# Kernel tuning notes

Hardware: AMD Instinct MI355X
Metric: run time of the kernel (lower is better)

Reference implementation:

```python
import jax, jax.numpy as jnp
import numpy as np

TOPK = 10
HID = 512
RHID = 150
CH = 32


def _gru(x, Wi, Wh, bi, bh):
    """torch nn.GRU (1 layer, batch_first) with gate order r,z,n. x: [B,T,D]."""
    H = Wh.shape[1]
    xi = x @ Wi.T + bi  # [B,T,3H] precompute input projections

    def step(h, xt):
        gh = h @ Wh.T + bh
        r = jax.nn.sigmoid(xt[:, :H] + gh[:, :H])
        z = jax.nn.sigmoid(xt[:, H:2 * H] + gh[:, H:2 * H])
        n = jnp.tanh(xt[:, 2 * H:] + r * gh[:, 2 * H:])
        h_new = (1.0 - z) * n + z * h
        return h_new, h_new

    h0 = jnp.zeros((x.shape[0], H), x.dtype)
    hT, ys = jax.lax.scan(step, h0, jnp.swapaxes(xi, 0, 1))
    return jnp.swapaxes(ys, 0, 1), hT


def reference(window, emb, w_init, w_root, arma_b, Wi1, Wh1, bi1, bh1,
              Wi2, Wh2, bi2, bh2, W_fc, b_fc):
    B, T, N = window.shape
    # --- SingleEmbedding (post-warmup): cosine similarity + per-row top-k ---
    Wn = emb / jnp.clip(jnp.linalg.norm(emb, axis=1, keepdims=True), 1e-8, None)
    A = Wn @ Wn.T
    A = A * (1.0 - jnp.eye(N, dtype=A.dtype))  # fill_diagonal_(0)
    A = jnp.maximum(A, 0.0)                    # clamp(0)
    vals, idx = jax.lax.top_k(A, TOPK)         # [N, TOPK]
    # zero-valued edges kept with weight 0: identical math (zero degree/message contribution)
    src = jnp.repeat(jnp.arange(N), TOPK)      # edge source = row i
    dst = idx.reshape(-1)                      # edge dest = col j
    attr = vals.reshape(-1)
    # --- batch edges over B (offset b*N), then over T (offset t*B*N), as in torch code ---
    boff = jnp.arange(B) * N
    bsrc = (src[None, :] + boff[:, None]).reshape(-1)   # [B*E]
    bdst = (dst[None, :] + boff[:, None]).reshape(-1)
    battr = jnp.tile(attr, B)
    toff = jnp.arange(T) * (B * N)
    fsrc = (bsrc[None, :] + toff[:, None]).reshape(-1)  # [T*B*E]
    fdst = (bdst[None, :] + toff[:, None]).reshape(-1)
    fattr = jnp.tile(battr, T)
    Ntot = B * N * T
    # node layout (b, n, t): flat row = (b*N + n)*T + t  (faithful to torch view order)
    x = jnp.transpose(window, (0, 2, 1)).reshape(Ntot, 1)
    # --- ARMAConv: 1 stack, 1 layer, GELU, gcn_norm without self-loops ---
    deg = jax.ops.segment_sum(fattr, fdst, num_segments=Ntot)
    dinv = jnp.where(deg > 0, jax.lax.rsqrt(jnp.where(deg > 0, deg, 1.0)), 0.0)
    enorm = dinv[fsrc] * fattr * dinv[fdst]
    h = x @ w_init                                            # [Ntot, CH]
    agg = jax.ops.segment_sum(h[fsrc] * enorm[:, None], fdst, num_segments=Ntot)
    out = jax.nn.gelu(agg + x @ w_root + arma_b, approximate=False)
    # --- add node embedding, GRU encode ---
    xt = out.reshape(B, N, T, CH).transpose(0, 2, 1, 3) + emb  # [B,T,N,CH]
    xt = xt.reshape(B, T, N * CH)
    _, h_end = _gru(xt, Wi1, Wh1, bi1, bh1)                   # [B, HID]
    # --- ReconstructionModel: repeat_interleave(T, dim=1).view(B,T,-1) then GRU+fc ---
    hrep = jnp.repeat(h_end, T, axis=1).reshape(B, T, HID)
    dec, _ = _gru(hrep, Wi2, Wh2, bi2, bh2)                   # [B,T,RHID]
    return dec @ W_fc.T + b_fc


def setup_inputs():
    key = jax.random.key(0)
    ks = jax.random.split(key, 10)
    B, T, N = 32, 100, 150
    d_in = N * CH
    return {
        "window": jax.random.normal(ks[0], (B, T, N), jnp.float32),
        "emb": jax.random.normal(ks[1], (N, CH), jnp.float32) * 0.3,
        "w_init": jax.random.normal(ks[2], (1, CH), jnp.float32) * 0.5,
        "w_root": jax.random.normal(ks[3], (1, CH), jnp.float32) * 0.5,
        "arma_b": jnp.zeros((CH,), jnp.float32),
        "Wi1": jax.random.normal(ks[4], (3 * HID, d_in), jnp.float32) * (1.0 / np.sqrt(d_in)),
        "Wh1": jax.random.normal(ks[5], (3 * HID, HID), jnp.float32) * (1.0 / np.sqrt(HID)),
        "bi1": jnp.zeros((3 * HID,), jnp.float32),
        "bh1": jnp.zeros((3 * HID,), jnp.float32),
        "Wi2": jax.random.normal(ks[6], (3 * RHID, HID), jnp.float32) * (1.0 / np.sqrt(HID)),
        "Wh2": jax.random.normal(ks[7], (3 * RHID, RHID), jnp.float32) * (1.0 / np.sqrt(RHID)),
        "bi2": jnp.zeros((3 * RHID,), jnp.float32),
        "bh2": jnp.zeros((3 * RHID,), jnp.float32),
        "W_fc": jax.random.normal(ks[8], (N, RHID), jnp.float32) * (1.0 / np.sqrt(RHID)),
        "b_fc": jnp.zeros((N,), jnp.float32),
    }
```

## Files before the change

### kernel.cpp

```cpp
#include <hip/hip_runtime.h>
#include <hip/hip_fp16.h>
#include <math.h>

typedef _Float16 f16;
typedef _Float16 half8 __attribute__((ext_vector_type(8)));
typedef _Float16 half4 __attribute__((ext_vector_type(4)));
typedef float float4v __attribute__((ext_vector_type(4)));
typedef float float2v __attribute__((ext_vector_type(2)));
typedef unsigned int uint4v __attribute__((ext_vector_type(4)));

#define AS1 __attribute__((address_space(1)))
#define AS3 __attribute__((address_space(3)))

constexpr size_t alup(size_t x){ return (x + 255) & ~(size_t)255; }
constexpr size_t OFF_MT   = 0;
constexpr size_t OFF_DEG  = alup(OFF_MT + 150*150*4);
constexpr size_t OFF_HT0  = alup(OFF_DEG + 150*4);
constexpr size_t OFF_HT1  = alup(OFF_HT0 + (size_t)32*512*4);
constexpr size_t OFF_WI2P = alup(OFF_HT1 + (size_t)32*512*4);
constexpr size_t OFF_WFCP = alup(OFF_WI2P + (size_t)512*512*2);
constexpr size_t OFF_DECB = alup(OFF_WFCP + (size_t)256*160*2);
constexpr size_t ZONE_END = alup(OFF_DECB + (size_t)3200*160*2);
constexpr size_t OFF_WN   = ZONE_END;
constexpr size_t OFF_EDST = alup(OFF_WN + 4800*4);
constexpr size_t OFF_EVAL = alup(OFF_EDST + 1500*4);
constexpr size_t OFF_XF   = alup(OFF_EVAL + 1500*4);
constexpr size_t OFF_SS   = alup(OFF_XF + (size_t)480000*4);
constexpr size_t OFF_XT   = alup(OFF_SS + (size_t)480000*4);
constexpr size_t OFF_WI1H = alup(OFF_XT + (size_t)3200*4800*2);
constexpr size_t OFF_XI1  = alup(OFF_WI1H + (size_t)1536*4800*2);
constexpr size_t OFF_U    = alup(OFF_XI1 + (size_t)3200*1536*4);
constexpr size_t OFF_XI2P = alup(OFF_U + (size_t)3200*512*2);

static __device__ __forceinline__ float fsig(float x){ return 1.0f/(1.0f + __expf(-x)); }
static __device__ __forceinline__ float ftanh(float x){
    x = fminf(fmaxf(x, -15.f), 15.f);
    float e = __expf(2.0f*x);
    return (e - 1.0f)/(e + 1.0f);
}
static __device__ __forceinline__ float sigmoidf_(float x){ return 1.0f/(1.0f+expf(-x)); }

__global__ void k_norm(const float* __restrict__ emb, float* __restrict__ WN) {
    int n = threadIdx.x;
    if (n < 150) {
        float s = 0.f;
        #pragma unroll
        for (int c = 0; c < 32; ++c) { float v = emb[n*32+c]; s += v*v; }
        float nrm = fmaxf(sqrtf(s), 1e-8f);
        float inv = 1.0f / nrm;
        #pragma unroll
        for (int c = 0; c < 32; ++c) WN[n*32+c] = emb[n*32+c] * inv;
    }
}

__global__ void k_topk(const float* __restrict__ WN, int* __restrict__ EDST,
                       float* __restrict__ EVAL, float* __restrict__ DEG) {
    __shared__ float WnT[32*152];
    __shared__ float As[160];
    int tid = threadIdx.x;
    int i = blockIdx.x;
    for (int idx = tid; idx < 4800; idx += 256) {
        int jj = idx >> 5, c = idx & 31;
        WnT[c*152 + jj] = WN[idx];
    }
    __syncthreads();
    int j = tid;
    if (j < 150) {
        float a = 0.f;
        #pragma unroll
        for (int c = 0; c < 32; ++c) a += WnT[c*152 + i] * WnT[c*152 + j];
        a = (j == i) ? 0.f : fmaxf(a, 0.f);
        As[j] = a;
    }
    __syncthreads();
    if (j < 150) {
        float aj = As[j];
        int cnt = 0;
        for (int m = 0; m < 150; ++m) {
            float am = As[m];
            cnt += (am > aj) || (am == aj && m < j);
        }
        if (cnt < 10) {
            EDST[i*10 + cnt] = j;
            EVAL[i*10 + cnt] = aj;
            atomicAdd(&DEG[j], aj);
        }
    }
}

__global__ void k_finalize(const int* __restrict__ EDST, const float* __restrict__ EVAL,
                           const float* __restrict__ DEG, float* __restrict__ MT) {
    __shared__ float dinv[160];
    int tid = threadIdx.x;
    if (tid < 150) {
        float d = DEG[tid];
        dinv[tid] = (d > 0.f) ? rsqrtf(d) : 0.f;
    }
    __syncthreads();
    for (int e = tid; e < 1500; e += 256) {
        int src = e / 10;
        int dst = EDST[e];
        MT[src*150 + dst] = dinv[src] * EVAL[e] * dinv[dst];
    }
}

__global__ void k_cvt_pad(const float* __restrict__ src, f16* __restrict__ dst,
                          int rows, int cols, int ldd) {
    long long idx = (long long)blockIdx.x * blockDim.x + threadIdx.x;
    long long n = (long long)rows * cols;
    if (idx >= n) return;
    if (ldd == cols) {
        dst[idx] = (f16)src[idx];
    } else {
        int r = (int)(idx / cols), c = (int)(idx % cols);
        dst[(size_t)r*ldd + c] = (f16)src[idx];
    }
}

__global__ void k_perm(const float* __restrict__ window, float* __restrict__ XF) {
    int idx = blockIdx.x * blockDim.x + threadIdx.x;
    if (idx >= 480000) return;
    float v = window[idx];
    int b = idx / 15000;
    int r = idx % 15000;
    int t = r / 150, n = r % 150;
    XF[b*15000 + n*100 + t] = v;
}

__global__ void k_conv(const float* __restrict__ XF, const float* __restrict__ MT,
                       float* __restrict__ SS) {
    __shared__ float xs[152];
    int tid = threadIdx.x;
    int base = blockIdx.x * 150;
    if (tid < 150) xs[tid] = XF[base + tid];
    __syncthreads();
    if (tid < 150) {
        float s = 0.f;
        for (int m = 0; m < 150; ++m) s += MT[m*150 + tid] * xs[m];
        SS[base + tid] = s;
    }
}

__global__ void k_xt(const float* __restrict__ SS, const float* __restrict__ XF,
                     const float* __restrict__ w_init, const float* __restrict__ w_root,
                     const float* __restrict__ arma_b, const float* __restrict__ emb,
                     f16* __restrict__ xt) {
    __shared__ float ssl[152];
    __shared__ float xfl[152];
    int tid = threadIdx.x;
    int bid = blockIdx.x;
    int b = bid / 100, t = bid % 100;
    if (tid < 150) {
        int f = b*15000 + tid*100 + t;
        ssl[tid] = SS[f];
        xfl[tid] = XF[f];
    }
    __syncthreads();
    for (int e = tid; e < 4800; e += 256) {
        int n = e >> 5, c = e & 31;
        float pre = ssl[n]*w_init[c] + xfl[n]*w_root[c] + arma_b[c];
        float g = 0.5f * pre * (1.0f + erff(pre * 0.70710678118654752f));
        xt[(size_t)bid*4800 + e] = (f16)(g + emb[e]);
    }
}

__global__ void k_gemm_f16(const f16* __restrict__ A, const f16* __restrict__ Bm,
                           const float* __restrict__ bias, float* __restrict__ C,
                           int K, int ldc, int nvalid, int ntn) {
    __shared__ f16 As[128*32];
    __shared__ f16 Bs[128*32];
    int tid = threadIdx.x;
    int lane = tid & 63, wave = tid >> 6;
    int wm = wave >> 1, wn = wave & 1;
    int tm = blockIdx.x / ntn, tn = blockIdx.x % ntn;
    int m0 = tm * 128, n0 = tn * 128;
    int lrow = lane & 15, quad = lane >> 4;

    float4v acc[4][4];
    #pragma unroll
    for (int mi = 0; mi < 4; ++mi)
        #pragma unroll
        for (int ni = 0; ni < 4; ++ni)
            acc[mi][ni] = (float4v){0.f, 0.f, 0.f, 0.f};

    for (int k0 = 0; k0 < K; k0 += 32) {
        #pragma unroll
        for (int i = 0; i < 2; ++i) {
            int chunk = i*256 + tid;
            int row = chunk >> 2, cq = chunk & 3;
            int cbase = chunk & ~63;
            const f16* ga = A + (size_t)(m0+row)*K + k0 + cq*8;
            __builtin_amdgcn_global_load_lds((const AS1 void*)ga, (AS3 void*)(As + cbase*8), 16, 0, 0);
            const f16* gb = Bm + (size_t)(n0+row)*K + k0 + cq*8;
            __builtin_amdgcn_global_load_lds((const AS1 void*)gb, (AS3 void*)(Bs + cbase*8), 16, 0, 0);
        }
        __syncthreads();
        half8 aF[4], bF[4];
        #pragma unroll
        for (int mi = 0; mi < 4; ++mi)
            aF[mi] = *(const half8*)&As[(wm*64 + mi*16 + lrow)*32 + quad*8];
        #pragma unroll
        for (int ni = 0; ni < 4; ++ni)
            bF[ni] = *(const half8*)&Bs[(wn*64 + ni*16 + lrow)*32 + quad*8];
        #pragma unroll
        for (int mi = 0; mi < 4; ++mi)
            #pragma unroll
            for (int ni = 0; ni < 4; ++ni)
                acc[mi][ni] = __builtin_amdgcn_mfma_f32_16x16x32_f16(aF[mi], bF[ni], acc[mi][ni], 0, 0, 0);
        __syncthreads();
    }

    #pragma unroll
    for (int ni = 0; ni < 4; ++ni) {
        int gcol = n0 + wn*64 + ni*16 + lrow;
        if (gcol >= nvalid) continue;
        float bv = bias[gcol];
        #pragma unroll
        for (int mi = 0; mi < 4; ++mi) {
            int growb = m0 + wm*64 + mi*16 + quad*4;
            #pragma unroll
            for (int r = 0; r < 4; ++r)
                C[(size_t)(growb + r)*ldc + gcol] = acc[mi][ni][r] + bv;
        }
    }
}

__global__ __launch_bounds__(256, 1)
void k_gru1(const float* __restrict__ xi1, const float* __restrict__ Wh1,
            const float* __restrict__ bh1, unsigned* __restrict__ ht0,
            unsigned* __restrict__ ht1) {
    __shared__ __align__(16) f16 hA[16*640];
    __shared__ float xis[192];
    __shared__ float ghs[192];
    int tid = threadIdx.x;
    int g = blockIdx.x & 15;
    int j = blockIdx.x >> 4;
    int b0 = g * 2;
    int lane = tid & 63, wave = tid >> 6;
    int lrow = lane & 15, quad = lane >> 4;

    half8 Bf0[16], Bf1[16];
    if (wave < 3) {
        #pragma unroll
        for (int tile = 0; tile < 2; ++tile) {
            int rr = (wave*2 + tile)*16 + lrow;
            int grow = (rr >> 5)*512 + (j << 5) + (rr & 31);
            const float* wp = Wh1 + (size_t)grow*512 + quad*8;
            #pragma unroll
            for (int k0 = 0; k0 < 16; ++k0) {
                float4v w0 = *(const float4v*)(wp + k0*32);
                float4v w1 = *(const float4v*)(wp + k0*32 + 4);
                half8 hb;
                hb[0]=(f16)w0[0]; hb[1]=(f16)w0[1]; hb[2]=(f16)w0[2]; hb[3]=(f16)w0[3];
                hb[4]=(f16)w1[0]; hb[5]=(f16)w1[1]; hb[6]=(f16)w1[2]; hb[7]=(f16)w1[3];
                if (tile == 0) Bf0[k0] = hb; else Bf1[k0] = hb;
            }
        }
    }

    float hold = 0.f, bhr = 0.f, bhz = 0.f, bhn = 0.f;
    if (tid < 64) {
        int col = (j << 5) + (tid & 31);
        bhr = bh1[col]; bhz = bh1[512 + col]; bhn = bh1[1024 + col];
    }
    float xr[3]; int xvi[3]; size_t xad[3];
    if (wave == 3) {
        int idx = tid - 192;
        #pragma unroll
        for (int q = 0; q < 3; ++q) {
            int vi = idx + 64*q; xvi[q] = vi;
            int bl = vi / 96, rr = vi % 96;
            int col = (rr >> 5)*512 + (j << 5) + (rr & 31);
            xad[q] = (size_t)((b0 + bl)*100)*1536 + col;
            xr[q] = xi1[xad[q]];
        }
    }
    int sbl = tid >> 7;
    int kb  = (tid & 127) << 2;

    for (int t = 0; t < 100; ++t) {
        const unsigned* cur = (t & 1) ? ht1 : ht0;
        unsigned* nxt = (t & 1) ? ht0 : ht1;
        {
            const unsigned* p = cur + (size_t)(b0 + sbl)*512 + kb;
            uint4v A4;
            unsigned tagw = (unsigned)t << 16;
            for (;;) {
                asm volatile("global_load_dwordx4 %0, %1, off sc0 sc1\n\ts_waitcnt vmcnt(0)"
                             : "=v"(A4) : "v"(p) : "memory");
                if ((A4[0] & 0xffff0000u) == tagw && (A4[1] & 0xffff0000u) == tagw &&
                    (A4[2] & 0xffff0000u) == tagw && (A4[3] & 0xffff0000u) == tagw) break;
                __builtin_amdgcn_s_sleep(1);
            }
            union { unsigned short s[4]; half4 h; } cv;
            cv.s[0] = (unsigned short)A4[0]; cv.s[1] = (unsigned short)A4[1];
            cv.s[2] = (unsigned short)A4[2]; cv.s[3] = (unsigned short)A4[3];
            *(half4*)&hA[(kb >> 5)*640 + sbl*40 + (kb & 31)] = cv.h;
        }
        __syncthreads();

        if (wave < 3) {
            float4v acc0 = (float4v){0.f,0.f,0.f,0.f}, acc1 = (float4v){0.f,0.f,0.f,0.f};
            const f16* aB = &hA[lrow*40 + quad*8];
            #pragma unroll
            for (int k0 = 0; k0 < 16; ++k0) {
                half8 a = *(const half8*)(aB + k0*640);
                acc0 = __builtin_amdgcn_mfma_f32_16x16x32_f16(a, Bf0[k0], acc0, 0, 0, 0);
                acc1 = __builtin_amdgcn_mfma_f32_16x16x32_f16(a, Bf1[k0], acc1, 0, 0, 0);
            }
            if (lane < 16) {
                int n0 = wave*2, n1 = n0 + 1;
                ghs[n0*16 + lane]      = acc0[0];
                ghs[96 + n0*16 + lane] = acc0[1];
                ghs[n1*16 + lane]      = acc1[0];
                ghs[96 + n1*16 + lane] = acc1[1];
            }
        } else {
            #pragma unroll
            for (int q = 0; q < 3; ++q) xis[xvi[q]] = xr[q];
            int tn = (t < 99) ? t + 1 : 99;
            #pragma unroll
            for (int q = 0; q < 3; ++q) xr[q] = xi1[xad[q] + (size_t)tn*1536];
        }
        __syncthreads();

        if (tid < 64) {
            int bl = tid >> 5, i = tid & 31;
            float gr = ghs[bl*96 + i]      + bhr;
            float gz = ghs[bl*96 + 32 + i] + bhz;
            float gn = ghs[bl*96 + 64 + i] + bhn;
            float r = fsig(xis[bl*96 + i] + gr);
            float z = fsig(xis[bl*96 + 32 + i] + gz);
            float n = ftanh(xis[bl*96 + 64 + i] + r*gn);
            float hnew = (1.f - z)*n + z*hold;
            hold = hnew;
            union { f16 h; unsigned short s; } hb; hb.h = (f16)hnew;
            unsigned pk = ((unsigned)(t + 1) << 16) | (unsigned)hb.s;
            __hip_atomic_store(nxt + (size_t)(b0 + bl)*512 + (j << 5) + i, pk,
                               __ATOMIC_RELAXED, __HIP_MEMORY_SCOPE_AGENT);
        }
    }
}

__global__ void k_build_u(const unsigned* __restrict__ ht0, f16* __restrict__ u) {
    int idx = blockIdx.x * blockDim.x + threadIdx.x;
    if (idx >= 32*100*512) return;
    int b = idx / 51200;
    int r = idx % 51200;
    int t = r >> 9, k = r & 511;
    union { unsigned short s; f16 h; } cv;
    cv.s = (unsigned short)ht0[(b << 9) + ((t*512 + k) / 100)];
    u[idx] = cv.h;
}

__global__ __launch_bounds__(512, 2)
void k_gru2(const float* __restrict__ xi2p, const float* __restrict__ Wh2,
            const float* __restrict__ bh2, f16* __restrict__ decb) {
    __shared__ float hs2[152];
    __shared__ float ghs2[456];
    __shared__ float xis2[456];
    int tid = threadIdx.x;
    int b = blockIdx.x;
    bool act = tid < 450;
    float2v w[75];
    float bhv = 0.f;
    if (act) {
        const float2v* wrow = (const float2v*)&Wh2[tid*150];
        #pragma unroll
        for (int k = 0; k < 75; ++k) w[k] = wrow[k];
        bhv = bh2[tid];
    }
    if (tid < 152) hs2[tid] = 0.f;
    size_t row0 = (size_t)b * 100 * 512;
    float xr = act ? xi2p[row0 + tid] : 0.f;
    __syncthreads();

    for (int t = 0; t < 100; ++t) {
        if (act) xis2[tid] = xr;
        __syncthreads();
        if (act) {
            float a = bhv;
            #pragma unroll
            for (int k = 0; k < 75; ++k)
                a += w[k][0] * hs2[2*k] + w[k][1] * hs2[2*k+1];
            ghs2[tid] = a;
        }
        int tn = (t < 99) ? t + 1 : 99;
        if (act) xr = xi2p[((size_t)b*100 + tn)*512 + tid];
        __syncthreads();
        if (tid < 150) {
            int i = tid;
            float r = fsig(xis2[i] + ghs2[i]);
            float z = fsig(xis2[150 + i] + ghs2[150 + i]);
            float n = ftanh(xis2[300 + i] + r * ghs2[300 + i]);
            float hnew = (1.f - z) * n + z * hs2[i];
            hs2[i] = hnew;
            decb[((size_t)b*100 + t)*160 + i] = (f16)hnew;
        }
        __syncthreads();
    }
}

extern "C" void kernel_launch(void* const* d_in, const int* in_sizes, int n_in,
                              void* d_out, int out_size, void* d_ws, size_t ws_size,
                              hipStream_t stream) {
    const float* window = (const float*)d_in[0];
    const float* emb    = (const float*)d_in[1];
    const float* w_init = (const float*)d_in[2];
    const float* w_root = (const float*)d_in[3];
    const float* arma_b = (const float*)d_in[4];
    const float* Wi1    = (const float*)d_in[5];
    const float* Wh1    = (const float*)d_in[6];
    const float* bi1    = (const float*)d_in[7];
    const float* bh1    = (const float*)d_in[8];
    const float* Wi2    = (const float*)d_in[9];
    const float* Wh2    = (const float*)d_in[10];
    const float* bi2    = (const float*)d_in[11];
    const float* bh2    = (const float*)d_in[12];
    const float* W_fc   = (const float*)d_in[13];
    const float* b_fc   = (const float*)d_in[14];
    float* out = (float*)d_out;

    char* ws = (char*)d_ws;
    float*    MT   = (float*)(ws + OFF_MT);
    float*    DEG  = (float*)(ws + OFF_DEG);
    unsigned* HT0  = (unsigned*)(ws + OFF_HT0);
    unsigned* HT1  = (unsigned*)(ws + OFF_HT1);
    f16*      WI2P = (f16*)  (ws + OFF_WI2P);
    f16*      WFCP = (f16*)  (ws + OFF_WFCP);
    f16*      DECB = (f16*)  (ws + OFF_DECB);
    float*    WN   = (float*)(ws + OFF_WN);
    int*      EDST = (int*)  (ws + OFF_EDST);
    float*    EVAL = (float*)(ws + OFF_EVAL);
    float*    XF   = (float*)(ws + OFF_XF);
    float*    SS   = (float*)(ws + OFF_SS);
    f16*      XT   = (f16*)  (ws + OFF_XT);
    f16*      WI1H = (f16*)  (ws + OFF_WI1H);
    float*    XI1  = (float*)(ws + OFF_XI1);
    f16*      UB   = (f16*)  (ws + OFF_U);
    float*    XI2P = (float*)(ws + OFF_XI2P);

    hipMemsetAsync(d_ws, 0, ZONE_END, stream);

    k_norm<<<1, 256, 0, stream>>>(emb, WN);
    k_topk<<<150, 256, 0, stream>>>(WN, EDST, EVAL, DEG);
    k_finalize<<<1, 256, 0, stream>>>(EDST, EVAL, DEG, MT);

    {
        long long n1 = (long long)1536*4800;
        k_cvt_pad<<<(unsigned)((n1 + 255)/256), 256, 0, stream>>>(Wi1, WI1H, 1536, 4800, 4800);
        long long n2 = (long long)450*512;
        k_cvt_pad<<<(unsigned)((n2 + 255)/256), 256, 0, stream>>>(Wi2, WI2P, 450, 512, 512);
        long long n3 = (long long)150*150;
        k_cvt_pad<<<(unsigned)((n3 + 255)/256), 256, 0, stream>>>(W_fc, WFCP, 150, 150, 160);
    }

    k_perm<<<(480000 + 255)/256, 256, 0, stream>>>(window, XF);
    k_conv<<<3200, 256, 0, stream>>>(XF, MT, SS);
    k_xt<<<3200, 256, 0, stream>>>(SS, XF, w_init, w_root, arma_b, emb, XT);

    k_gemm_f16<<<25*12, 256, 0, stream>>>(XT, WI1H, bi1, XI1, 4800, 1536, 1536, 12);

    k_gru1<<<256, 256, 0, stream>>>(XI1, Wh1, bh1, HT0, HT1);

    k_build_u<<<(32*100*512 + 255)/256, 256, 0, stream>>>(HT0, UB);

    k_gemm_f16<<<25*4, 256, 0, stream>>>(UB, WI2P, bi2, XI2P, 512, 512, 450, 4);

    k_gru2<<<32, 512, 0, stream>>>(XI2P, Wh2, bh2, DECB);

    k_gemm_f16<<<25*2, 256, 0, stream>>>(DECB, WFCP, b_fc, out, 160, 150, 150, 2);

    (void)in_sizes; (void)n_in; (void)out_size; (void)ws_size;
}
```

Before: 625.1 us.

## Fuse prep kernels, widen GEMM K-tile, store GRU input projections in fp16

Folds the embedding normalization into the top-k kernel and merges finalize, weight conversion and window permutation into one prep launch, cutting launch count. The GEMM now uses a 64-wide K tile with an M-major block order, and its outputs XI1/XI2 are written as fp16 instead of fp32, halving traffic for the GRU input reads. GRU1 keeps per-thread prefetched fp16 inputs in registers instead of a dedicated loader wave, and splits its MFMA accumulation into two chains. The changes add fp16 rounding of the input projections and pad the decoder buffers to 192.

```diff
diff --git a/kernel.cpp b/kernel.cpp
--- a/kernel.cpp
+++ b/kernel.cpp
@@ -19,18 +19,17 @@
 constexpr size_t OFF_HT1  = alup(OFF_HT0 + (size_t)32*512*4);
 constexpr size_t OFF_WI2P = alup(OFF_HT1 + (size_t)32*512*4);
 constexpr size_t OFF_WFCP = alup(OFF_WI2P + (size_t)512*512*2);
-constexpr size_t OFF_DECB = alup(OFF_WFCP + (size_t)256*160*2);
-constexpr size_t ZONE_END = alup(OFF_DECB + (size_t)3200*160*2);
-constexpr size_t OFF_WN   = ZONE_END;
-constexpr size_t OFF_EDST = alup(OFF_WN + 4800*4);
+constexpr size_t OFF_DECB = alup(OFF_WFCP + (size_t)256*192*2);
+constexpr size_t ZONE_END = alup(OFF_DECB + (size_t)3200*192*2);
+constexpr size_t OFF_EDST = ZONE_END;
 constexpr size_t OFF_EVAL = alup(OFF_EDST + 1500*4);
 constexpr size_t OFF_XF   = alup(OFF_EVAL + 1500*4);
 constexpr size_t OFF_SS   = alup(OFF_XF + (size_t)480000*4);
 constexpr size_t OFF_XT   = alup(OFF_SS + (size_t)480000*4);
 constexpr size_t OFF_WI1H = alup(OFF_XT + (size_t)3200*4800*2);
 constexpr size_t OFF_XI1  = alup(OFF_WI1H + (size_t)1536*4800*2);
-constexpr size_t OFF_U    = alup(OFF_XI1 + (size_t)3200*1536*4);
-constexpr size_t OFF_XI2P = alup(OFF_U + (size_t)3200*512*2);
+constexpr size_t OFF_U    = alup(OFF_XI1 + (size_t)3200*1536*2);
+constexpr size_t OFF_XI2  = alup(OFF_U + (size_t)3200*512*2);
 
 static __device__ __forceinline__ float fsig(float x){ return 1.0f/(1.0f + __expf(-x)); }
 static __device__ __forceinline__ float ftanh(float x){
@@ -38,30 +37,29 @@
     float e = __expf(2.0f*x);
     return (e - 1.0f)/(e + 1.0f);
 }
-static __device__ __forceinline__ float sigmoidf_(float x){ return 1.0f/(1.0f+expf(-x)); }
-
-__global__ void k_norm(const float* __restrict__ emb, float* __restrict__ WN) {
-    int n = threadIdx.x;
-    if (n < 150) {
-        float s = 0.f;
-        #pragma unroll
-        for (int c = 0; c < 32; ++c) { float v = emb[n*32+c]; s += v*v; }
-        float nrm = fmaxf(sqrtf(s), 1e-8f);
-        float inv = 1.0f / nrm;
-        #pragma unroll
-        for (int c = 0; c < 32; ++c) WN[n*32+c] = emb[n*32+c] * inv;
-    }
-}
-
-__global__ void k_topk(const float* __restrict__ WN, int* __restrict__ EDST,
+
+__global__ void k_topk(const float* __restrict__ emb, int* __restrict__ EDST,
                        float* __restrict__ EVAL, float* __restrict__ DEG) {
     __shared__ float WnT[32*152];
+    __shared__ float invn[160];
     __shared__ float As[160];
     int tid = threadIdx.x;
     int i = blockIdx.x;
     for (int idx = tid; idx < 4800; idx += 256) {
         int jj = idx >> 5, c = idx & 31;
-        WnT[c*152 + jj] = WN[idx];
+        WnT[c*152 + jj] = emb[idx];
+    }
+    __syncthreads();
+    if (tid < 150) {
+        float s = 0.f;
+        #pragma unroll
+        for (int c = 0; c < 32; ++c) { float v = WnT[c*152 + tid]; s += v*v; }
+        invn[tid] = 1.0f / fmaxf(sqrtf(s), 1e-8f);
+    }
+    __syncthreads();
+    for (int idx = tid; idx < 4800; idx += 256) {
+        int jj = idx >> 5, c = idx & 31;
+        WnT[c*152 + jj] *= invn[jj];
     }
     __syncthreads();
     int j = tid;
@@ -88,43 +86,45 @@
     }
 }
 
-__global__ void k_finalize(const int* __restrict__ EDST, const float* __restrict__ EVAL,
-                           const float* __restrict__ DEG, float* __restrict__ MT) {
-    __shared__ float dinv[160];
-    int tid = threadIdx.x;
-    if (tid < 150) {
-        float d = DEG[tid];
-        dinv[tid] = (d > 0.f) ? rsqrtf(d) : 0.f;
-    }
-    __syncthreads();
-    for (int e = tid; e < 1500; e += 256) {
-        int src = e / 10;
-        int dst = EDST[e];
-        MT[src*150 + dst] = dinv[src] * EVAL[e] * dinv[dst];
-    }
-}
-
-__global__ void k_cvt_pad(const float* __restrict__ src, f16* __restrict__ dst,
-                          int rows, int cols, int ldd) {
-    long long idx = (long long)blockIdx.x * blockDim.x + threadIdx.x;
-    long long n = (long long)rows * cols;
-    if (idx >= n) return;
-    if (ldd == cols) {
-        dst[idx] = (f16)src[idx];
+__global__ void k_prep(const int* __restrict__ EDST, const float* __restrict__ EVAL,
+                       const float* __restrict__ DEG, float* __restrict__ MT,
+                       const float* __restrict__ Wi1, f16* __restrict__ WI1H,
+                       const float* __restrict__ Wi2, f16* __restrict__ WI2P,
+                       const float* __restrict__ W_fc, f16* __restrict__ WFCP,
+                       const float* __restrict__ window, float* __restrict__ XF) {
+    int b = blockIdx.x, tid = threadIdx.x;
+    if (b == 0) {
+        __shared__ float dinv[160];
+        if (tid < 150) {
+            float d = DEG[tid];
+            dinv[tid] = (d > 0.f) ? rsqrtf(d) : 0.f;
+        }
+        __syncthreads();
+        for (int e = tid; e < 1500; e += 256) {
+            int src = e / 10;
+            int dst = EDST[e];
+            MT[src*150 + dst] = dinv[src] * EVAL[e] * dinv[dst];
+        }
+    } else if (b < 28801) {
+        int idx = (b - 1)*256 + tid;
+        WI1H[idx] = (f16)Wi1[idx];
+    } else if (b < 29701) {
+        int idx = (b - 28801)*256 + tid;
+        WI2P[idx] = (f16)Wi2[idx];
+    } else if (b < 29789) {
+        int idx = (b - 29701)*256 + tid;
+        if (idx < 22500) {
+            int r = idx / 150, c = idx % 150;
+            WFCP[r*192 + c] = (f16)W_fc[idx];
+        }
     } else {
-        int r = (int)(idx / cols), c = (int)(idx % cols);
-        dst[(size_t)r*ldd + c] = (f16)src[idx];
-    }
-}
-
-__global__ void k_perm(const float* __restrict__ window, float* __restrict__ XF) {
-    int idx = blockIdx.x * blockDim.x + threadIdx.x;
-    if (idx >= 480000) return;
-    float v = window[idx];
-    int b = idx / 15000;
-    int r = idx % 15000;
-    int t = r / 150, n = r % 150;
-    XF[b*15000 + n*100 + t] = v;
+        int idx = (b - 29789)*256 + tid;
+        float v = window[idx];
+        int bb = idx / 15000;
+        int r = idx % 15000;
+        int t = r / 150, n = r % 150;
+        XF[bb*15000 + n*100 + t] = v;
+    }
 }
 
 __global__ void k_conv(const float* __restrict__ XF, const float* __restrict__ MT,
@@ -164,15 +164,16 @@
     }
 }
 
-__global__ void k_gemm_f16(const f16* __restrict__ A, const f16* __restrict__ Bm,
-                           const float* __restrict__ bias, float* __restrict__ C,
-                           int K, int ldc, int nvalid, int ntn) {
-    __shared__ f16 As[128*32];
-    __shared__ f16 Bs[128*32];
+template <typename TC>
+__global__ void k_gemm(const f16* __restrict__ A, const f16* __restrict__ Bm,
+                       const float* __restrict__ bias, TC* __restrict__ C,
+                       int K, int ldc, int nvalid, int ntm) {
+    __shared__ f16 As[128*64];
+    __shared__ f16 Bs[128*64];
     int tid = threadIdx.x;
     int lane = tid & 63, wave = tid >> 6;
     int wm = wave >> 1, wn = wave & 1;
-    int tm = blockIdx.x / ntn, tn = blockIdx.x % ntn;
+    int tm = blockIdx.x % ntm, tn = blockIdx.x / ntm;
     int m0 = tm * 128, n0 = tn * 128;
     int lrow = lane & 15, quad = lane >> 4;
 
@@ -183,30 +184,33 @@
         for (int ni = 0; ni < 4; ++ni)
             acc[mi][ni] = (float4v){0.f, 0.f, 0.f, 0.f};
 
-    for (int k0 = 0; k0 < K; k0 += 32) {
-        #pragma unroll
-        for (int i = 0; i < 2; ++i) {
-            int chunk = i*256 + tid;
-            int row = chunk >> 2, cq = chunk & 3;
-            int cbase = chunk & ~63;
+    for (int k0 = 0; k0 < K; k0 += 64) {
+        #pragma unroll
+        for (int i = 0; i < 4; ++i) {
+            int cid = i*256 + tid;
+            int row = cid >> 3, cq = cid & 7;
+            int cbase = cid & ~63;
             const f16* ga = A + (size_t)(m0+row)*K + k0 + cq*8;
             __builtin_amdgcn_global_load_lds((const AS1 void*)ga, (AS3 void*)(As + cbase*8), 16, 0, 0);
             const f16* gb = Bm + (size_t)(n0+row)*K + k0 + cq*8;
             __builtin_amdgcn_global_load_lds((const AS1 void*)gb, (AS3 void*)(Bs + cbase*8), 16, 0, 0);
         }
         __syncthreads();
-        half8 aF[4], bF[4];
-        #pragma unroll
-        for (int mi = 0; mi < 4; ++mi)
-            aF[mi] = *(const half8*)&As[(wm*64 + mi*16 + lrow)*32 + quad*8];
-        #pragma unroll
-        for (int ni = 0; ni < 4; ++ni)
-            bF[ni] = *(const half8*)&Bs[(wn*64 + ni*16 + lrow)*32 + quad*8];
-        #pragma unroll
-        for (int mi = 0; mi < 4; ++mi)
+        #pragma unroll
+        for (int kk = 0; kk < 2; ++kk) {
+            half8 aF[4], bF[4];
+            #pragma unroll
+            for (int mi = 0; mi < 4; ++mi)
+                aF[mi] = *(const half8*)&As[(wm*64 + mi*16 + lrow)*64 + kk*32 + quad*8];
             #pragma unroll
             for (int ni = 0; ni < 4; ++ni)
-                acc[mi][ni] = __builtin_amdgcn_mfma_f32_16x16x32_f16(aF[mi], bF[ni], acc[mi][ni], 0, 0, 0);
+                bF[ni] = *(const half8*)&Bs[(wn*64 + ni*16 + lrow)*64 + kk*32 + quad*8];
+            #pragma unroll
+            for (int mi = 0; mi < 4; ++mi)
+                #pragma unroll
+                for (int ni = 0; ni < 4; ++ni)
+                    acc[mi][ni] = __builtin_amdgcn_mfma_f32_16x16x32_f16(aF[mi], bF[ni], acc[mi][ni], 0, 0, 0);
+        }
         __syncthreads();
     }
 
@@ -220,17 +224,16 @@
             int growb = m0 + wm*64 + mi*16 + quad*4;
             #pragma unroll
             for (int r = 0; r < 4; ++r)
-                C[(size_t)(growb + r)*ldc + gcol] = acc[mi][ni][r] + bv;
+                C[(size_t)(growb + r)*ldc + gcol] = (TC)(acc[mi][ni][r] + bv);
         }
     }
 }
 
 __global__ __launch_bounds__(256, 1)
-void k_gru1(const float* __restrict__ xi1, const float* __restrict__ Wh1,
+void k_gru1(const f16* __restrict__ xi1, const float* __restrict__ Wh1,
             const float* __restrict__ bh1, unsigned* __restrict__ ht0,
             unsigned* __restrict__ ht1) {
     __shared__ __align__(16) f16 hA[16*640];
-    __shared__ float xis[192];
     __shared__ float ghs[192];
     int tid = threadIdx.x;
     int g = blockIdx.x & 15;
@@ -259,21 +262,14 @@
     }
 
     float hold = 0.f, bhr = 0.f, bhz = 0.f, bhn = 0.f;
+    f16 xir = (f16)0.f, xiz = (f16)0.f, xin = (f16)0.f;
+    size_t xb = 0;
     if (tid < 64) {
-        int col = (j << 5) + (tid & 31);
+        int bl = tid >> 5, i = tid & 31;
+        int col = (j << 5) + i;
         bhr = bh1[col]; bhz = bh1[512 + col]; bhn = bh1[1024 + col];
-    }
-    float xr[3]; int xvi[3]; size_t xad[3];
-    if (wave == 3) {
-        int idx = tid - 192;
-        #pragma unroll
-        for (int q = 0; q < 3; ++q) {
-            int vi = idx + 64*q; xvi[q] = vi;
-            int bl = vi / 96, rr = vi % 96;
-            int col = (rr >> 5)*512 + (j << 5) + (rr & 31);
-            xad[q] = (size_t)((b0 + bl)*100)*1536 + col;
-            xr[q] = xi1[xad[q]];
-        }
+        xb = (size_t)((b0 + bl)*100)*1536 + col;
+        xir = xi1[xb]; xiz = xi1[xb + 512]; xin = xi1[xb + 1024];
     }
     int sbl = tid >> 7;
     int kb  = (tid & 127) << 2;
@@ -300,38 +296,39 @@
         __syncthreads();
 
         if (wave < 3) {
-            float4v acc0 = (float4v){0.f,0.f,0.f,0.f}, acc1 = (float4v){0.f,0.f,0.f,0.f};
+            float4v a0a = (float4v){0.f,0.f,0.f,0.f}, a0b = a0a, a1a = a0a, a1b = a0a;
             const f16* aB = &hA[lrow*40 + quad*8];
             #pragma unroll
-            for (int k0 = 0; k0 < 16; ++k0) {
-                half8 a = *(const half8*)(aB + k0*640);
-                acc0 = __builtin_amdgcn_mfma_f32_16x16x32_f16(a, Bf0[k0], acc0, 0, 0, 0);
-                acc1 = __builtin_amdgcn_mfma_f32_16x16x32_f16(a, Bf1[k0], acc1, 0, 0, 0);
+            for (int k0 = 0; k0 < 16; k0 += 2) {
+                half8 a0 = *(const half8*)(aB + k0*640);
+                half8 a1 = *(const half8*)(aB + (k0+1)*640);
+                a0a = __builtin_amdgcn_mfma_f32_16x16x32_f16(a0, Bf0[k0], a0a, 0, 0, 0);
+                a1a = __builtin_amdgcn_mfma_f32_16x16x32_f16(a0, Bf1[k0], a1a, 0, 0, 0);
+                a0b = __builtin_amdgcn_mfma_f32_16x16x32_f16(a1, Bf0[k0+1], a0b, 0, 0, 0);
+                a1b = __builtin_amdgcn_mfma_f32_16x16x32_f16(a1, Bf1[k0+1], a1b, 0, 0, 0);
             }
             if (lane < 16) {
                 int n0 = wave*2, n1 = n0 + 1;
-                ghs[n0*16 + lane]      = acc0[0];
-                ghs[96 + n0*16 + lane] = acc0[1];
-                ghs[n1*16 + lane]      = acc1[0];
-                ghs[96 + n1*16 + lane] = acc1[1];
+                ghs[n0*16 + lane]      = a0a[0] + a0b[0];
+                ghs[96 + n0*16 + lane] = a0a[1] + a0b[1];
+                ghs[n1*16 + lane]      = a1a[0] + a1b[0];
+                ghs[96 + n1*16 + lane] = a1a[1] + a1b[1];
             }
-        } else {
-            #pragma unroll
-            for (int q = 0; q < 3; ++q) xis[xvi[q]] = xr[q];
-            int tn = (t < 99) ? t + 1 : 99;
-            #pragma unroll
-            for (int q = 0; q < 3; ++q) xr[q] = xi1[xad[q] + (size_t)tn*1536];
         }
         __syncthreads();
 
         if (tid < 64) {
             int bl = tid >> 5, i = tid & 31;
+            float xr_ = (float)xir, xz_ = (float)xiz, xn_ = (float)xin;
+            int tn = (t < 99) ? t + 1 : 99;
+            size_t xo = xb + (size_t)tn*1536;
+            xir = xi1[xo]; xiz = xi1[xo + 512]; xin = xi1[xo + 1024];
             float gr = ghs[bl*96 + i]      + bhr;
             float gz = ghs[bl*96 + 32 + i] + bhz;
             float gn = ghs[bl*96 + 64 + i] + bhn;
-            float r = fsig(xis[bl*96 + i] + gr);
-            float z = fsig(xis[bl*96 + 32 + i] + gz);
-            float n = ftanh(xis[bl*96 + 64 + i] + r*gn);
+            float r = fsig(xr_ + gr);
+            float z = fsig(xz_ + gz);
+            float n = ftanh(xn_ + r*gn);
             float hnew = (1.f - z)*n + z*hold;
             hold = hnew;
             union { f16 h; unsigned short s; } hb; hb.h = (f16)hnew;
@@ -354,7 +351,7 @@
 }
 
 __global__ __launch_bounds__(512, 2)
-void k_gru2(const float* __restrict__ xi2p, const float* __restrict__ Wh2,
+void k_gru2(const f16* __restrict__ xi2, const float* __restrict__ Wh2,
             const float* __restrict__ bh2, f16* __restrict__ decb) {
     __shared__ float hs2[152];
     __shared__ float ghs2[456];
@@ -372,7 +369,7 @@
     }
     if (tid < 152) hs2[tid] = 0.f;
     size_t row0 = (size_t)b * 100 * 512;
-    float xr = act ? xi2p[row0 + tid] : 0.f;
+    float xr = act ? (float)xi2[row0 + tid] : 0.f;
     __syncthreads();
 
     for (int t = 0; t < 100; ++t) {
@@ -386,7 +383,7 @@
             ghs2[tid] = a;
         }
         int tn = (t < 99) ? t + 1 : 99;
-        if (act) xr = xi2p[((size_t)b*100 + tn)*512 + tid];
+        if (act) xr = (float)xi2[((size_t)b*100 + tn)*512 + tid];
         __syncthreads();
         if (tid < 150) {
             int i = tid;
@@ -395,7 +392,7 @@
             float n = ftanh(xis2[300 + i] + r * ghs2[300 + i]);
             float hnew = (1.f - z) * n + z * hs2[i];
             hs2[i] = hnew;
-            decb[((size_t)b*100 + t)*160 + i] = (f16)hnew;
+            decb[((size_t)b*100 + t)*192 + i] = (f16)hnew;
         }
         __syncthreads();
     }
@@ -429,47 +426,37 @@
     f16*      WI2P = (f16*)  (ws + OFF_WI2P);
     f16*      WFCP = (f16*)  (ws + OFF_WFCP);
     f16*      DECB = (f16*)  (ws + OFF_DECB);
-    float*    WN   = (float*)(ws + OFF_WN);
     int*      EDST = (int*)  (ws + OFF_EDST);
     float*    EVAL = (float*)(ws + OFF_EVAL);
     float*    XF   = (float*)(ws + OFF_XF);
     float*    SS   = (float*)(ws + OFF_SS);
     f16*      XT   = (f16*)  (ws + OFF_XT);
     f16*      WI1H = (f16*)  (ws + OFF_WI1H);
-    float*    XI1  = (float*)(ws + OFF_XI1);
+    f16*      XI1H = (f16*)  (ws + OFF_XI1);
     f16*      UB   = (f16*)  (ws + OFF_U);
-    float*    XI2P = (float*)(ws + OFF_XI2P);
+    f16*      XI2H = (f16*)  (ws + OFF_XI2);
 
     hipMemsetAsync(d_ws, 0, ZONE_END, stream);
 
-    k_norm<<<1, 256, 0, stream>>>(emb, WN);
-    k_topk<<<150, 256, 0, stream>>>(WN, EDST, EVAL, DEG);
-    k_finalize<<<1, 256, 0, stream>>>(EDST, EVAL, DEG, MT);
-
-    {
-        long long n1 = (long long)1536*4800;
-        k_cvt_pad<<<(unsigned)((n1 + 255)/256), 256, 0, stream>>>(Wi1, WI1H, 1536, 4800, 4800);
-        long long n2 = (long long)450*512;
-        k_cvt_pad<<<(unsigned)((n2 + 255)/256), 256, 0, stream>>>(Wi2, WI2P, 450, 512, 512);
-        long long n3 = (long long)150*150;
-        k_cvt_pad<<<(unsigned)((n3 + 255)/256), 256, 0, stream>>>(W_fc, WFCP, 150, 150, 160);
-    }
-
-    k_perm<<<(480000 + 255)/256, 256, 0, stream>>>(window, XF);
+    k_topk<<<150, 256, 0, stream>>>(emb, EDST, EVAL, DEG);
+
+    k_prep<<<31664, 256, 0, stream>>>(EDST, EVAL, DEG, MT,
+                                      Wi1, WI1H, Wi2, WI2P, W_fc, WFCP, window, XF);
+
     k_conv<<<3200, 256, 0, stream>>>(XF, MT, SS);
     k_xt<<<3200, 256, 0, stream>>>(SS, XF, w_init, w_root, arma_b, emb, XT);
 
-    k_gemm_f16<<<25*12, 256, 0, stream>>>(XT, WI1H, bi1, XI1, 4800, 1536, 1536, 12);
-
-    k_gru1<<<256, 256, 0, stream>>>(XI1, Wh1, bh1, HT0, HT1);
+    k_gemm<f16><<<25*12, 256, 0, stream>>>(XT, WI1H, bi1, XI1H, 4800, 1536, 1536, 25);
+
+    k_gru1<<<256, 256, 0, stream>>>(XI1H, Wh1, bh1, HT0, HT1);
 
     k_build_u<<<(32*100*512 + 255)/256, 256, 0, stream>>>(HT0, UB);
 
-    k_gemm_f16<<<25*4, 256, 0, stream>>>(UB, WI2P, bi2, XI2P, 512, 512, 450, 4);
-
-    k_gru2<<<32, 512, 0, stream>>>(XI2P, Wh2, bh2, DECB);
-
-    k_gemm_f16<<<25*2, 256, 0, stream>>>(DECB, WFCP, b_fc, out, 160, 150, 150, 2);
+    k_gemm<f16><<<25*4, 256, 0, stream>>>(UB, WI2P, bi2, XI2H, 512, 512, 450, 25);
+
+    k_gru2<<<32, 512, 0, stream>>>(XI2H, Wh2, bh2, DECB);
+
+    k_gemm<float><<<25*2, 256, 0, stream>>>(DECB, WFCP, b_fc, out, 192, 150, 150, 25);
 
     (void)in_sizes; (void)n_in; (void)out_size; (void)ws_size;
 }
```

Measured after the change: 615.0 us. Within noise of the previous version (-1.6%).
